# Kernel tuning notes

Measured on AMD Instinct MI355X. Metric: run time of the kernel, lower is better.

Reference implementation:

```python
import jax, jax.numpy as jnp
import numpy as np

N_NODES = 50000
N_EDGES = 1000000


def _edge_conv(x, src, dst, W, b, n_nodes):
    """PyG EdgeConv: msg = nn(cat([x_i, x_j - x_i])), aggr=max over incoming edges."""
    xi = x[dst]                      # [E, C] target features
    xj = x[src]                      # [E, C] source features
    m = jnp.concatenate([xi, xj - xi], axis=-1)          # [E, 2C]
    m = jax.nn.relu(m @ W + b)                           # [E, C_out]
    out = jax.ops.segment_max(m, dst, num_segments=n_nodes)  # [N, C_out]
    # empty segments produce -inf; PyG fills with 0
    return jnp.where(jnp.isfinite(out), out, 0.0)


def setup_inputs() -> dict:
    key = jax.random.key(0)
    ks = jax.random.split(key, 12)
    x = jax.random.normal(ks[0], (N_NODES, 3), dtype=jnp.float32)
    edge_index = jax.random.randint(ks[1], (2, N_EDGES), 0, N_NODES, dtype=jnp.int64)

    def lin(k, fan_in, fan_out):
        s = 1.0 / np.sqrt(fan_in)
        kw, kb = jax.random.split(k)
        W = jax.random.uniform(kw, (fan_in, fan_out), jnp.float32, -s, s)
        b = jax.random.uniform(kb, (fan_out,), jnp.float32, -s, s)
        return W, b

    W1, b1 = lin(ks[2], 6, 64)       # conv1 MLP([3*2, 64])
    W2, b2 = lin(ks[3], 128, 128)    # conv2 MLP([64*2, 128])
    W3, b3 = lin(ks[4], 256, 512)    # conv3 MLP([128*2, 512])
    W4, b4 = lin(ks[5], 512, 256)    # lin1 MLP([512, 256])
    W5, b5 = lin(ks[6], 256, 3)      # lin1 final Linear(256, 3)
    return {"x": x, "edge_index": edge_index,
            "W1": W1, "b1": b1, "W2": W2, "b2": b2, "W3": W3, "b3": b3,
            "W4": W4, "b4": b4, "W5": W5, "b5": b5}


def reference(x, edge_index, W1, b1, W2, b2, W3, b3, W4, b4, W5, b5):
    src = edge_index[0]  # x_j
    dst = edge_index[1]  # x_i (aggregation target)
    n = x.shape[0]
    x1 = _edge_conv(x, src, dst, W1, b1, n)    # [N, 64]
    x2 = _edge_conv(x1, src, dst, W2, b2, n)   # [N, 128]
    x3 = _edge_conv(x2, src, dst, W3, b3, n)   # [N, 512]
    x4 = jax.nn.relu(x3 @ W4 + b4) @ W5 + b5   # [N, 3]
    return x + x4
```

## Files before the change

### kernel.cpp

```cpp
#include <hip/hip_runtime.h>

static constexpr int NN = 50000;
static constexpr int NE = 1000000;

typedef short bf16x8 __attribute__((ext_vector_type(8)));
typedef float f32x4 __attribute__((ext_vector_type(4)));

__device__ inline float bf2f_raw(unsigned short u) {
    return __uint_as_float(((unsigned int)u) << 16);
}
__device__ inline unsigned short f2bf(float f) {
    unsigned int u = __float_as_uint(f);
    u += 0x7fffu + ((u >> 16) & 1u);
    return (unsigned short)(u >> 16);
}
__device__ inline void fmax2(float& a0, float& a1, unsigned int v) {
    a0 = fmaxf(a0, bf2f_raw((unsigned short)(v & 0xffffu)));
    a1 = fmaxf(a1, bf2f_raw((unsigned short)(v >> 16)));
}
__device__ inline unsigned int pack2(float f0, float f1) {
    return (unsigned int)f2bf(f0) | ((unsigned int)f2bf(f1) << 16);
}
__device__ inline unsigned int addrelu2(unsigned int a, float t0, float t1) {
    float f0 = fmaxf(bf2f_raw((unsigned short)(a & 0xffffu)) + t0, 0.f);
    float f1 = fmaxf(bf2f_raw((unsigned short)(a >> 16)) + t1, 0.f);
    return pack2(f0, f1);
}


__global__ void hist_kernel(const int* __restrict__ dst, int* __restrict__ deg) {
    int e = blockIdx.x * blockDim.x + threadIdx.x;
    if (e < NE) atomicAdd(&deg[dst[e]], 1);
}

__global__ __launch_bounds__(1024) void scan_kernel(const int* __restrict__ deg,
                                                    int* __restrict__ rowstart) {
    __shared__ int wave_sums[16];
    __shared__ int carry_s;
    int tid = threadIdx.x;
    int lane = tid & 63;
    int wave = tid >> 6;
    if (tid == 0) carry_s = 0;
    __syncthreads();
    for (int base = 0; base < NN; base += 1024) {
        int idx = base + tid;
        int v = (idx < NN) ? deg[idx] : 0;
        int x = v;
        #pragma unroll
        for (int off = 1; off < 64; off <<= 1) {
            int y = __shfl_up(x, off);
            if (lane >= off) x += y;
        }
        if (lane == 63) wave_sums[wave] = x;
        __syncthreads();
        if (wave == 0 && lane < 16) {
            int s = wave_sums[lane];
            #pragma unroll
            for (int off = 1; off < 16; off <<= 1) {
                int y = __shfl_up(s, off);
                if (lane >= off) s += y;
            }
            wave_sums[lane] = s;
        }
        __syncthreads();
        int wave_off = wave ? wave_sums[wave - 1] : 0;
        int chunk_total = wave_sums[15];
        int carry = carry_s;
        if (idx < NN) rowstart[idx] = carry + wave_off + x - v;
        __syncthreads();
        if (tid == 0) carry_s = carry + chunk_total;
        __syncthreads();
    }
    if (tid == 0) rowstart[NN] = carry_s;
}

__global__ void scatter_kernel(const int* __restrict__ src, const int* __restrict__ dst,
                               const int* __restrict__ rowstart, int* __restrict__ cursor,
                               int* __restrict__ csr) {
    int e = blockIdx.x * blockDim.x + threadIdx.x;
    if (e < NE) {
        int d = dst[e];
        int pos = atomicAdd(&cursor[d], 1);
        csr[rowstart[d] + pos] = src[e];
    }
}


template<int CIN, int COUT>
__global__ void prep_split_t_kernel(const float* __restrict__ W,
                                    unsigned short* __restrict__ Wtbt,
                                    unsigned short* __restrict__ Wbt) {
    int t = blockIdx.x * blockDim.x + threadIdx.x;
    if (t >= CIN * COUT) return;
    int k = t / COUT, c = t % COUT;
    float wt = W[k * COUT + c];
    float wb = W[(CIN + k) * COUT + c];
    Wtbt[c * CIN + k] = f2bf(wt - wb);
    Wbt[c * CIN + k] = f2bf(wb);
}

template<int K, int N>
__global__ void prep_t_kernel(const float* __restrict__ W, unsigned short* __restrict__ Wt) {
    int t = blockIdx.x * blockDim.x + threadIdx.x;
    if (t >= K * N) return;
    int k = t / N, n = t % N;
    Wt[n * K + k] = f2bf(W[k * N + n]);
}


__global__ void conv1_s_kernel(const float* __restrict__ x, const float* __restrict__ W1,
                               unsigned short* __restrict__ s) {
    int t = blockIdx.x * blockDim.x + threadIdx.x;
    int i = t >> 6, c = t & 63;
    if (i >= NN) return;
    float v = x[i * 3 + 0] * W1[3 * 64 + c] + x[i * 3 + 1] * W1[4 * 64 + c] +
              x[i * 3 + 2] * W1[5 * 64 + c];
    s[t] = f2bf(v);
}


__global__ __launch_bounds__(256) void edge_fused_conv1_kernel(
    const unsigned short* __restrict__ s1, const int* __restrict__ rowstart,
    const int* __restrict__ csr, const float* __restrict__ x,
    const float* __restrict__ W1, const float* __restrict__ b1,
    unsigned short* __restrict__ x1) {
    int wid = (blockIdx.x * 256 + threadIdx.x) >> 6;
    int lane = threadIdx.x & 63;
    if (wid >= NN) return;
    int e0 = __builtin_amdgcn_readfirstlane(rowstart[wid]);
    int e1 = __builtin_amdgcn_readfirstlane(rowstart[wid + 1]);
    int h = lane >> 5, c0 = (lane & 31) * 2;
    float t0 = -INFINITY, t1 = -INFINITY;
    const unsigned short* sb = s1 + c0;
    int nedge = e1 - e0;
    for (int base = 0; base < nedge; base += 64) {
        int rem = nedge - base;
        int myj = csr[(lane < rem) ? (e0 + base + lane) : e0];
        int cnt = rem < 64 ? rem : 64;
        int cp = (cnt + 7) & ~7;
        for (int q = 0; q < cp; q += 8) {
            int j0 = __shfl(myj, q + 0 + h);
            int j1 = __shfl(myj, q + 2 + h);
            int j2 = __shfl(myj, q + 4 + h);
            int j3 = __shfl(myj, q + 6 + h);
            unsigned int v0 = *(const unsigned int*)(sb + (size_t)j0 * 64);
            unsigned int v1 = *(const unsigned int*)(sb + (size_t)j1 * 64);
            unsigned int v2 = *(const unsigned int*)(sb + (size_t)j2 * 64);
            unsigned int v3 = *(const unsigned int*)(sb + (size_t)j3 * 64);
            fmax2(t0, t1, v0);
            fmax2(t0, t1, v1);
            fmax2(t0, t1, v2);
            fmax2(t0, t1, v3);
        }
    }
    t0 = fmaxf(t0, __shfl_xor(t0, 32));
    t1 = fmaxf(t1, __shfl_xor(t1, 32));
    if (h == 0) {
        float x0 = x[wid * 3 + 0], xv1 = x[wid * 3 + 1], xv2 = x[wid * 3 + 2];
        int c1 = c0 + 1;
        float a0 = x0 * (W1[c0] - W1[192 + c0]) + xv1 * (W1[64 + c0] - W1[256 + c0]) +
                   xv2 * (W1[128 + c0] - W1[320 + c0]) + b1[c0];
        float a1 = x0 * (W1[c1] - W1[192 + c1]) + xv1 * (W1[64 + c1] - W1[256 + c1]) +
                   xv2 * (W1[128 + c1] - W1[320 + c1]) + b1[c1];
        *(unsigned int*)(x1 + (size_t)wid * 64 + c0) =
            pack2(fmaxf(a0 + t0, 0.f), fmaxf(a1 + t1, 0.f));
    }
}


__global__ __launch_bounds__(256) void edge_fused128_kernel(
    const unsigned short* __restrict__ as, const int* __restrict__ rowstart,
    const int* __restrict__ csr, unsigned short* __restrict__ xout) {
    int wid = (blockIdx.x * 256 + threadIdx.x) >> 6;
    int lane = threadIdx.x & 63;
    if (wid >= NN) return;
    int e0 = __builtin_amdgcn_readfirstlane(rowstart[wid]);
    int e1 = __builtin_amdgcn_readfirstlane(rowstart[wid + 1]);
    float t0 = -INFINITY, t1 = -INFINITY;
    const unsigned short* sb = as + 128 + (size_t)lane * 2;
    int nedge = e1 - e0;
    for (int base = 0; base < nedge; base += 64) {
        int rem = nedge - base;
        int myj = csr[(lane < rem) ? (e0 + base + lane) : e0];
        int cnt = rem < 64 ? rem : 64;
        int cp = (cnt + 7) & ~7;
        for (int q = 0; q < cp; q += 8) {
            int j0 = __shfl(myj, q + 0), j1 = __shfl(myj, q + 1);
            int j2 = __shfl(myj, q + 2), j3 = __shfl(myj, q + 3);
            int j4 = __shfl(myj, q + 4), j5 = __shfl(myj, q + 5);
            int j6 = __shfl(myj, q + 6), j7 = __shfl(myj, q + 7);
            unsigned int v0 = *(const unsigned int*)(sb + (size_t)j0 * 256);
            unsigned int v1 = *(const unsigned int*)(sb + (size_t)j1 * 256);
            unsigned int v2 = *(const unsigned int*)(sb + (size_t)j2 * 256);
            unsigned int v3 = *(const unsigned int*)(sb + (size_t)j3 * 256);
            unsigned int v4 = *(const unsigned int*)(sb + (size_t)j4 * 256);
            unsigned int v5 = *(const unsigned int*)(sb + (size_t)j5 * 256);
            unsigned int v6 = *(const unsigned int*)(sb + (size_t)j6 * 256);
            unsigned int v7 = *(const unsigned int*)(sb + (size_t)j7 * 256);
            fmax2(t0, t1, v0); fmax2(t0, t1, v1);
            fmax2(t0, t1, v2); fmax2(t0, t1, v3);
            fmax2(t0, t1, v4); fmax2(t0, t1, v5);
            fmax2(t0, t1, v6); fmax2(t0, t1, v7);
        }
    }
    unsigned int av = *(const unsigned int*)(as + (size_t)wid * 256 + lane * 2);
    *(unsigned int*)(xout + (size_t)wid * 128 + lane * 2) = addrelu2(av, t0, t1);
}


__global__ __launch_bounds__(256) void edge_fused512_kernel(
    const unsigned short* __restrict__ as, const int* __restrict__ rowstart,
    const int* __restrict__ csr, unsigned short* __restrict__ xout) {
    int wid = (blockIdx.x * 256 + threadIdx.x) >> 6;
    int lane = threadIdx.x & 63;
    if (wid >= NN) return;
    int e0 = __builtin_amdgcn_readfirstlane(rowstart[wid]);
    int e1 = __builtin_amdgcn_readfirstlane(rowstart[wid + 1]);
    float acc[8];
    #pragma unroll
    for (int v = 0; v < 8; ++v) acc[v] = -INFINITY;
    const unsigned short* sb = as + 512 + (size_t)lane * 8;
    int nedge = e1 - e0;
    for (int base = 0; base < nedge; base += 64) {
        int rem = nedge - base;
        int myj = csr[(lane < rem) ? (e0 + base + lane) : e0];
        int cnt = rem < 64 ? rem : 64;
        int cp = (cnt + 7) & ~7;
        for (int q = 0; q < cp; q += 8) {
            int j0 = __shfl(myj, q + 0), j1 = __shfl(myj, q + 1);
            int j2 = __shfl(myj, q + 2), j3 = __shfl(myj, q + 3);
            int j4 = __shfl(myj, q + 4), j5 = __shfl(myj, q + 5);
            int j6 = __shfl(myj, q + 6), j7 = __shfl(myj, q + 7);
            uint4 v0 = *(const uint4*)(sb + (size_t)j0 * 1024);
            uint4 v1 = *(const uint4*)(sb + (size_t)j1 * 1024);
            uint4 v2 = *(const uint4*)(sb + (size_t)j2 * 1024);
            uint4 v3 = *(const uint4*)(sb + (size_t)j3 * 1024);
            uint4 v4 = *(const uint4*)(sb + (size_t)j4 * 1024);
            uint4 v5 = *(const uint4*)(sb + (size_t)j5 * 1024);
            uint4 v6 = *(const uint4*)(sb + (size_t)j6 * 1024);
            uint4 v7 = *(const uint4*)(sb + (size_t)j7 * 1024);
            fmax2(acc[0], acc[1], v0.x); fmax2(acc[2], acc[3], v0.y);
            fmax2(acc[4], acc[5], v0.z); fmax2(acc[6], acc[7], v0.w);
            fmax2(acc[0], acc[1], v1.x); fmax2(acc[2], acc[3], v1.y);
            fmax2(acc[4], acc[5], v1.z); fmax2(acc[6], acc[7], v1.w);
            fmax2(acc[0], acc[1], v2.x); fmax2(acc[2], acc[3], v2.y);
            fmax2(acc[4], acc[5], v2.z); fmax2(acc[6], acc[7], v2.w);
            fmax2(acc[0], acc[1], v3.x); fmax2(acc[2], acc[3], v3.y);
            fmax2(acc[4], acc[5], v3.z); fmax2(acc[6], acc[7], v3.w);
            fmax2(acc[0], acc[1], v4.x); fmax2(acc[2], acc[3], v4.y);
            fmax2(acc[4], acc[5], v4.z); fmax2(acc[6], acc[7], v4.w);
            fmax2(acc[0], acc[1], v5.x); fmax2(acc[2], acc[3], v5.y);
            fmax2(acc[4], acc[5], v5.z); fmax2(acc[6], acc[7], v5.w);
            fmax2(acc[0], acc[1], v6.x); fmax2(acc[2], acc[3], v6.y);
            fmax2(acc[4], acc[5], v6.z); fmax2(acc[6], acc[7], v6.w);
            fmax2(acc[0], acc[1], v7.x); fmax2(acc[2], acc[3], v7.y);
            fmax2(acc[4], acc[5], v7.z); fmax2(acc[6], acc[7], v7.w);
        }
    }
    uint4 av = *(const uint4*)(as + (size_t)wid * 1024 + lane * 8);
    uint4 o;
    o.x = addrelu2(av.x, acc[0], acc[1]);
    o.y = addrelu2(av.y, acc[2], acc[3]);
    o.z = addrelu2(av.z, acc[4], acc[5]);
    o.w = addrelu2(av.w, acc[6], acc[7]);
    *(uint4*)(xout + (size_t)wid * 512 + lane * 8) = o;
}


template<bool RELU>
__global__ __launch_bounds__(256) void mfma_gemm_kernel(
    const unsigned short* __restrict__ A, const unsigned short* __restrict__ Bt,
    const float* __restrict__ bias, int bias_n,
    unsigned short* __restrict__ C, int M, int N, int K) {
    __shared__ __align__(16) unsigned short Asl[128 * 40];
    __shared__ __align__(16) unsigned short Bsl[128 * 40];
    int tid = threadIdx.x;
    int mbase = blockIdx.y * 128, nbase = blockIdx.x * 128;
    int wave = tid >> 6, lane = tid & 63;
    int wm = (wave >> 1) * 64, wn = (wave & 1) * 64;
    int quad = lane >> 4, l16 = lane & 15;
    f32x4 acc[4][4] = {};
    for (int kb = 0; kb < K; kb += 32) {
        #pragma unroll
        for (int h = 0; h < 2; ++h) {
            int c = tid + h * 256;
            int r = c >> 2, kk = (c & 3) * 8;
            uint4 va = make_uint4(0u, 0u, 0u, 0u);
            int gr = mbase + r;
            if (gr < M) va = *(const uint4*)&A[(size_t)gr * K + kb + kk];
            *(uint4*)&Asl[r * 40 + kk] = va;
            uint4 vb = *(const uint4*)&Bt[(size_t)(nbase + r) * K + kb + kk];
            *(uint4*)&Bsl[r * 40 + kk] = vb;
        }
        __syncthreads();
        bf16x8 af[4], bfr[4];
        #pragma unroll
        for (int tt = 0; tt < 4; ++tt) {
            af[tt]  = *(const bf16x8*)&Asl[(wm + tt * 16 + l16) * 40 + quad * 8];
            bfr[tt] = *(const bf16x8*)&Bsl[(wn + tt * 16 + l16) * 40 + quad * 8];
        }
        #pragma unroll
        for (int mt = 0; mt < 4; ++mt)
            #pragma unroll
            for (int nt = 0; nt < 4; ++nt)
                acc[mt][nt] = __builtin_amdgcn_mfma_f32_16x16x32_bf16(
                    af[mt], bfr[nt], acc[mt][nt], 0, 0, 0);
        __syncthreads();
    }
    #pragma unroll
    for (int mt = 0; mt < 4; ++mt) {
        #pragma unroll
        for (int r = 0; r < 4; ++r) {
            int row = mbase + wm + mt * 16 + quad * 4 + r;
            if (row >= M) continue;
            #pragma unroll
            for (int nt = 0; nt < 4; ++nt) {
                int col = nbase + wn + nt * 16 + l16;
                float v = acc[mt][nt][r];
                if (col < bias_n) v += bias[col];
                if (RELU) v = fmaxf(v, 0.f);
                C[(size_t)row * N + col] = f2bf(v);
            }
        }
    }
}


__global__ void final_kernel(const unsigned short* __restrict__ h4,
                             const float* __restrict__ W5, const float* __restrict__ b5,
                             const float* __restrict__ x, float* __restrict__ out) {
    int gt = blockIdx.x * blockDim.x + threadIdx.x;
    int node = gt >> 6;
    int lane = gt & 63;
    if (node >= NN) return;
    ushort4 hv = ((const ushort4*)(h4 + (size_t)node * 256))[lane];
    float hj[4] = {bf2f_raw(hv.x), bf2f_raw(hv.y), bf2f_raw(hv.z), bf2f_raw(hv.w)};
    float acc0 = 0.f, acc1 = 0.f, acc2 = 0.f;
    #pragma unroll
    for (int j = 0; j < 4; ++j) {
        int k = lane * 4 + j;
        acc0 += hj[j] * W5[k * 3 + 0];
        acc1 += hj[j] * W5[k * 3 + 1];
        acc2 += hj[j] * W5[k * 3 + 2];
    }
    #pragma unroll
    for (int off = 32; off; off >>= 1) {
        acc0 += __shfl_down(acc0, off);
        acc1 += __shfl_down(acc1, off);
        acc2 += __shfl_down(acc2, off);
    }
    if (lane == 0) {
        out[node * 3 + 0] = x[node * 3 + 0] + acc0 + b5[0];
        out[node * 3 + 1] = x[node * 3 + 1] + acc1 + b5[1];
        out[node * 3 + 2] = x[node * 3 + 2] + acc2 + b5[2];
    }
}

__global__ void fallback_copy_kernel(const float* __restrict__ x, float* __restrict__ out) {
    int t = blockIdx.x * blockDim.x + threadIdx.x;
    if (t < NN * 3) out[t] = x[t];
}


extern "C" void kernel_launch(void* const* d_in, const int* in_sizes, int n_in,
                              void* d_out, int out_size, void* d_ws, size_t ws_size,
                              hipStream_t stream) {
    const float* x  = (const float*)d_in[0];
    const int*   ei = (const int*)d_in[1];
    const float* W1 = (const float*)d_in[2];
    const float* b1 = (const float*)d_in[3];
    const float* W2 = (const float*)d_in[4];
    const float* b2 = (const float*)d_in[5];
    const float* W3 = (const float*)d_in[6];
    const float* b3 = (const float*)d_in[7];
    const float* W4 = (const float*)d_in[8];
    const float* b4 = (const float*)d_in[9];
    const float* W5 = (const float*)d_in[10];
    const float* b5 = (const float*)d_in[11];
    float* out = (float*)d_out;

    char* p = (char*)d_ws;
    auto alloc = [&](size_t bytes) -> void* {
        void* r = (void*)p;
        p += (bytes + 255) & ~(size_t)255;
        return r;
    };
    int* deg      = (int*)alloc((size_t)NN * 4);
    int* rowstart = (int*)alloc((size_t)(NN + 1) * 4);
    int* cursor   = (int*)alloc((size_t)NN * 4);
    int* csr      = (int*)alloc((size_t)NE * 4);
    unsigned short* Bt2 = (unsigned short*)alloc(256 * 64 * 2);
    unsigned short* Bt3 = (unsigned short*)alloc(1024 * 128 * 2);
    unsigned short* W4t = (unsigned short*)alloc(256 * 512 * 2);
    unsigned short* x1 = (unsigned short*)alloc((size_t)NN * 64 * 2);
    unsigned short* x2 = (unsigned short*)alloc((size_t)NN * 128 * 2);
    unsigned short* x3 = (unsigned short*)alloc((size_t)NN * 512 * 2);
    unsigned short* as_slab = (unsigned short*)alloc((size_t)NN * 1024 * 2);
    size_t need = (size_t)(p - (char*)d_ws);
    if (ws_size < need) {
        fallback_copy_kernel<<<(NN * 3 + 255) / 256, 256, 0, stream>>>(x, out);
        return;
    }
    unsigned short* s1 = as_slab;
    unsigned short* h4 = as_slab;

    const int* src = ei;
    const int* dst = ei + NE;

    hipMemsetAsync(deg, 0, (size_t)NN * 4, stream);
    hipMemsetAsync(cursor, 0, (size_t)NN * 4, stream);
    hist_kernel<<<(NE + 255) / 256, 256, 0, stream>>>(dst, deg);
    scan_kernel<<<1, 1024, 0, stream>>>(deg, rowstart);
    scatter_kernel<<<(NE + 255) / 256, 256, 0, stream>>>(src, dst, rowstart, cursor, csr);

    prep_split_t_kernel<64, 128><<<32, 256, 0, stream>>>(W2, Bt2, Bt2 + 128 * 64);
    prep_split_t_kernel<128, 512><<<256, 256, 0, stream>>>(W3, Bt3, Bt3 + 512 * 128);
    prep_t_kernel<512, 256><<<512, 256, 0, stream>>>(W4, W4t);

    conv1_s_kernel<<<NN * 64 / 256, 256, 0, stream>>>(x, W1, s1);
    edge_fused_conv1_kernel<<<12500, 256, 0, stream>>>(s1, rowstart, csr, x, W1, b1, x1);

    mfma_gemm_kernel<false><<<dim3(2, 391), 256, 0, stream>>>(
        x1, Bt2, b2, 128, as_slab, NN, 256, 64);
    edge_fused128_kernel<<<12500, 256, 0, stream>>>(as_slab, rowstart, csr, x2);

    mfma_gemm_kernel<false><<<dim3(8, 391), 256, 0, stream>>>(
        x2, Bt3, b3, 512, as_slab, NN, 1024, 128);
    edge_fused512_kernel<<<12500, 256, 0, stream>>>(as_slab, rowstart, csr, x3);

    mfma_gemm_kernel<true><<<dim3(2, 391), 256, 0, stream>>>(
        x3, W4t, b4, 256, h4, NN, 256, 512);

    final_kernel<<<NN / 4, 256, 0, stream>>>(h4, W5, b5, x, out);
}
```

Baseline: 634.3 us.

## Fuse final W5 projection into W4 GEMM epilogue and merge setup kernels

Fuses the last linear layer (W5) into the epilogue of the W4 MFMA GEMM. Each 128-column tile reduces its ReLU outputs against W5 and atomically adds into an output pre-initialised with x+b5, which removes the h4 write/read and the separate final kernel. It also merges the three weight-prep kernels into one launch, moves the cursor zeroing into the scan kernel to drop a memset, and halves the gather unroll in the 512-wide edge kernel. The cost is float atomics on the output, which make summation order nondeterministic, and possibly less memory-level parallelism in the edge gather.

```diff
diff --git a/kernel.cpp b/kernel.cpp
--- a/kernel.cpp
+++ b/kernel.cpp
@@ -28,18 +28,27 @@
 }
 
 
+__global__ void init_out_kernel(const float* __restrict__ x, const float* __restrict__ b5,
+                                float* __restrict__ out) {
+    int t = blockIdx.x * blockDim.x + threadIdx.x;
+    if (t < NN * 3) out[t] = x[t] + b5[t % 3];
+}
+
+
 __global__ void hist_kernel(const int* __restrict__ dst, int* __restrict__ deg) {
     int e = blockIdx.x * blockDim.x + threadIdx.x;
     if (e < NE) atomicAdd(&deg[dst[e]], 1);
 }
 
 __global__ __launch_bounds__(1024) void scan_kernel(const int* __restrict__ deg,
-                                                    int* __restrict__ rowstart) {
+                                                    int* __restrict__ rowstart,
+                                                    int* __restrict__ cursor) {
     __shared__ int wave_sums[16];
     __shared__ int carry_s;
     int tid = threadIdx.x;
     int lane = tid & 63;
     int wave = tid >> 6;
+    for (int i = tid; i < NN; i += 1024) cursor[i] = 0;
     if (tid == 0) carry_s = 0;
     __syncthreads();
     for (int base = 0; base < NN; base += 1024) {
@@ -86,25 +95,30 @@
 }
 
 
-template<int CIN, int COUT>
-__global__ void prep_split_t_kernel(const float* __restrict__ W,
-                                    unsigned short* __restrict__ Wtbt,
-                                    unsigned short* __restrict__ Wbt) {
+__global__ void prep_all_kernel(const float* __restrict__ W2, const float* __restrict__ W3,
+                                const float* __restrict__ W4,
+                                unsigned short* __restrict__ Bt2,
+                                unsigned short* __restrict__ Bt3,
+                                unsigned short* __restrict__ W4t) {
     int t = blockIdx.x * blockDim.x + threadIdx.x;
-    if (t >= CIN * COUT) return;
-    int k = t / COUT, c = t % COUT;
-    float wt = W[k * COUT + c];
-    float wb = W[(CIN + k) * COUT + c];
-    Wtbt[c * CIN + k] = f2bf(wt - wb);
-    Wbt[c * CIN + k] = f2bf(wb);
-}
-
-template<int K, int N>
-__global__ void prep_t_kernel(const float* __restrict__ W, unsigned short* __restrict__ Wt) {
-    int t = blockIdx.x * blockDim.x + threadIdx.x;
-    if (t >= K * N) return;
-    int k = t / N, n = t % N;
-    Wt[n * K + k] = f2bf(W[k * N + n]);
+    if (t < 8192) {
+        int k = t / 128, c = t % 128;
+        float wt = W2[k * 128 + c];
+        float wb = W2[(64 + k) * 128 + c];
+        Bt2[c * 64 + k] = f2bf(wt - wb);
+        Bt2[(128 + c) * 64 + k] = f2bf(wb);
+    } else if (t < 8192 + 65536) {
+        int u = t - 8192;
+        int k = u / 512, c = u % 512;
+        float wt = W3[k * 512 + c];
+        float wb = W3[(128 + k) * 512 + c];
+        Bt3[c * 128 + k] = f2bf(wt - wb);
+        Bt3[(512 + c) * 128 + k] = f2bf(wb);
+    } else if (t < 8192 + 65536 + 131072) {
+        int u = t - 8192 - 65536;
+        int k = u / 256, n = u % 256;
+        W4t[n * 512 + k] = f2bf(W4[k * 256 + n]);
+    }
 }
 
 
@@ -225,20 +239,14 @@
         int rem = nedge - base;
         int myj = csr[(lane < rem) ? (e0 + base + lane) : e0];
         int cnt = rem < 64 ? rem : 64;
-        int cp = (cnt + 7) & ~7;
-        for (int q = 0; q < cp; q += 8) {
+        int cp = (cnt + 3) & ~3;
+        for (int q = 0; q < cp; q += 4) {
             int j0 = __shfl(myj, q + 0), j1 = __shfl(myj, q + 1);
             int j2 = __shfl(myj, q + 2), j3 = __shfl(myj, q + 3);
-            int j4 = __shfl(myj, q + 4), j5 = __shfl(myj, q + 5);
-            int j6 = __shfl(myj, q + 6), j7 = __shfl(myj, q + 7);
             uint4 v0 = *(const uint4*)(sb + (size_t)j0 * 1024);
             uint4 v1 = *(const uint4*)(sb + (size_t)j1 * 1024);
             uint4 v2 = *(const uint4*)(sb + (size_t)j2 * 1024);
             uint4 v3 = *(const uint4*)(sb + (size_t)j3 * 1024);
-            uint4 v4 = *(const uint4*)(sb + (size_t)j4 * 1024);
-            uint4 v5 = *(const uint4*)(sb + (size_t)j5 * 1024);
-            uint4 v6 = *(const uint4*)(sb + (size_t)j6 * 1024);
-            uint4 v7 = *(const uint4*)(sb + (size_t)j7 * 1024);
             fmax2(acc[0], acc[1], v0.x); fmax2(acc[2], acc[3], v0.y);
             fmax2(acc[4], acc[5], v0.z); fmax2(acc[6], acc[7], v0.w);
             fmax2(acc[0], acc[1], v1.x); fmax2(acc[2], acc[3], v1.y);
@@ -247,14 +255,6 @@
             fmax2(acc[4], acc[5], v2.z); fmax2(acc[6], acc[7], v2.w);
             fmax2(acc[0], acc[1], v3.x); fmax2(acc[2], acc[3], v3.y);
             fmax2(acc[4], acc[5], v3.z); fmax2(acc[6], acc[7], v3.w);
-            fmax2(acc[0], acc[1], v4.x); fmax2(acc[2], acc[3], v4.y);
-            fmax2(acc[4], acc[5], v4.z); fmax2(acc[6], acc[7], v4.w);
-            fmax2(acc[0], acc[1], v5.x); fmax2(acc[2], acc[3], v5.y);
-            fmax2(acc[4], acc[5], v5.z); fmax2(acc[6], acc[7], v5.w);
-            fmax2(acc[0], acc[1], v6.x); fmax2(acc[2], acc[3], v6.y);
-            fmax2(acc[4], acc[5], v6.z); fmax2(acc[6], acc[7], v6.w);
-            fmax2(acc[0], acc[1], v7.x); fmax2(acc[2], acc[3], v7.y);
-            fmax2(acc[4], acc[5], v7.z); fmax2(acc[6], acc[7], v7.w);
         }
     }
     uint4 av = *(const uint4*)(as + (size_t)wid * 1024 + lane * 8);
@@ -267,7 +267,6 @@
 }
 
 
-template<bool RELU>
 __global__ __launch_bounds__(256) void mfma_gemm_kernel(
     const unsigned short* __restrict__ A, const unsigned short* __restrict__ Bt,
     const float* __restrict__ bias, int bias_n,
@@ -318,7 +317,6 @@
                 int col = nbase + wn + nt * 16 + l16;
                 float v = acc[mt][nt][r];
                 if (col < bias_n) v += bias[col];
-                if (RELU) v = fmaxf(v, 0.f);
                 C[(size_t)row * N + col] = f2bf(v);
             }
         }
@@ -326,33 +324,79 @@
 }
 
 
-__global__ void final_kernel(const unsigned short* __restrict__ h4,
-                             const float* __restrict__ W5, const float* __restrict__ b5,
-                             const float* __restrict__ x, float* __restrict__ out) {
-    int gt = blockIdx.x * blockDim.x + threadIdx.x;
-    int node = gt >> 6;
-    int lane = gt & 63;
-    if (node >= NN) return;
-    ushort4 hv = ((const ushort4*)(h4 + (size_t)node * 256))[lane];
-    float hj[4] = {bf2f_raw(hv.x), bf2f_raw(hv.y), bf2f_raw(hv.z), bf2f_raw(hv.w)};
-    float acc0 = 0.f, acc1 = 0.f, acc2 = 0.f;
+__global__ __launch_bounds__(256) void mfma_gemm_w5_kernel(
+    const unsigned short* __restrict__ A, const unsigned short* __restrict__ Bt,
+    const float* __restrict__ b4, const float* __restrict__ W5,
+    float* __restrict__ out, int M, int K) {
+    __shared__ __align__(16) unsigned short Asl[128 * 40];
+    __shared__ __align__(16) unsigned short Bsl[128 * 40];
+    int tid = threadIdx.x;
+    int mbase = blockIdx.y * 128, nbase = blockIdx.x * 128;
+    int wave = tid >> 6, lane = tid & 63;
+    int wm = (wave >> 1) * 64, wn = (wave & 1) * 64;
+    int quad = lane >> 4, l16 = lane & 15;
+    f32x4 acc[4][4] = {};
+    for (int kb = 0; kb < K; kb += 32) {
+        #pragma unroll
+        for (int h = 0; h < 2; ++h) {
+            int c = tid + h * 256;
+            int r = c >> 2, kk = (c & 3) * 8;
+            uint4 va = make_uint4(0u, 0u, 0u, 0u);
+            int gr = mbase + r;
+            if (gr < M) va = *(const uint4*)&A[(size_t)gr * K + kb + kk];
+            *(uint4*)&Asl[r * 40 + kk] = va;
+            uint4 vb = *(const uint4*)&Bt[(size_t)(nbase + r) * K + kb + kk];
+            *(uint4*)&Bsl[r * 40 + kk] = vb;
+        }
+        __syncthreads();
+        bf16x8 af[4], bfr[4];
+        #pragma unroll
+        for (int tt = 0; tt < 4; ++tt) {
+            af[tt]  = *(const bf16x8*)&Asl[(wm + tt * 16 + l16) * 40 + quad * 8];
+            bfr[tt] = *(const bf16x8*)&Bsl[(wn + tt * 16 + l16) * 40 + quad * 8];
+        }
+        #pragma unroll
+        for (int mt = 0; mt < 4; ++mt)
+            #pragma unroll
+            for (int nt = 0; nt < 4; ++nt)
+                acc[mt][nt] = __builtin_amdgcn_mfma_f32_16x16x32_bf16(
+                    af[mt], bfr[nt], acc[mt][nt], 0, 0, 0);
+        __syncthreads();
+    }
+    float w5r[4][3], b4v[4];
     #pragma unroll
-    for (int j = 0; j < 4; ++j) {
-        int k = lane * 4 + j;
-        acc0 += hj[j] * W5[k * 3 + 0];
-        acc1 += hj[j] * W5[k * 3 + 1];
-        acc2 += hj[j] * W5[k * 3 + 2];
+    for (int nt = 0; nt < 4; ++nt) {
+        int col = nbase + wn + nt * 16 + l16;
+        b4v[nt] = b4[col];
+        w5r[nt][0] = W5[col * 3 + 0];
+        w5r[nt][1] = W5[col * 3 + 1];
+        w5r[nt][2] = W5[col * 3 + 2];
     }
     #pragma unroll
-    for (int off = 32; off; off >>= 1) {
-        acc0 += __shfl_down(acc0, off);
-        acc1 += __shfl_down(acc1, off);
-        acc2 += __shfl_down(acc2, off);
-    }
-    if (lane == 0) {
-        out[node * 3 + 0] = x[node * 3 + 0] + acc0 + b5[0];
-        out[node * 3 + 1] = x[node * 3 + 1] + acc1 + b5[1];
-        out[node * 3 + 2] = x[node * 3 + 2] + acc2 + b5[2];
+    for (int mt = 0; mt < 4; ++mt) {
+        #pragma unroll
+        for (int r = 0; r < 4; ++r) {
+            int row = mbase + wm + mt * 16 + quad * 4 + r;
+            float p0 = 0.f, p1 = 0.f, p2 = 0.f;
+            #pragma unroll
+            for (int nt = 0; nt < 4; ++nt) {
+                float h = fmaxf(acc[mt][nt][r] + b4v[nt], 0.f);
+                p0 += h * w5r[nt][0];
+                p1 += h * w5r[nt][1];
+                p2 += h * w5r[nt][2];
+            }
+            #pragma unroll
+            for (int m = 8; m; m >>= 1) {
+                p0 += __shfl_xor(p0, m);
+                p1 += __shfl_xor(p1, m);
+                p2 += __shfl_xor(p2, m);
+            }
+            if (l16 == 0 && row < M) {
+                atomicAdd(&out[row * 3 + 0], p0);
+                atomicAdd(&out[row * 3 + 1], p1);
+                atomicAdd(&out[row * 3 + 2], p2);
+            }
+        }
     }
 }
 
@@ -402,34 +446,30 @@
         return;
     }
     unsigned short* s1 = as_slab;
-    unsigned short* h4 = as_slab;
 
     const int* src = ei;
     const int* dst = ei + NE;
 
+    init_out_kernel<<<(NN * 3 + 255) / 256, 256, 0, stream>>>(x, b5, out);
+
     hipMemsetAsync(deg, 0, (size_t)NN * 4, stream);
-    hipMemsetAsync(cursor, 0, (size_t)NN * 4, stream);
     hist_kernel<<<(NE + 255) / 256, 256, 0, stream>>>(dst, deg);
-    scan_kernel<<<1, 1024, 0, stream>>>(deg, rowstart);
+    scan_kernel<<<1, 1024, 0, stream>>>(deg, rowstart, cursor);
     scatter_kernel<<<(NE + 255) / 256, 256, 0, stream>>>(src, dst, rowstart, cursor, csr);
 
-    prep_split_t_kernel<64, 128><<<32, 256, 0, stream>>>(W2, Bt2, Bt2 + 128 * 64);
-    prep_split_t_kernel<128, 512><<<256, 256, 0, stream>>>(W3, Bt3, Bt3 + 512 * 128);
-    prep_t_kernel<512, 256><<<512, 256, 0, stream>>>(W4, W4t);
+    prep_all_kernel<<<800, 256, 0, stream>>>(W2, W3, W4, Bt2, Bt3, W4t);
 
     conv1_s_kernel<<<NN * 64 / 256, 256, 0, stream>>>(x, W1, s1);
     edge_fused_conv1_kernel<<<12500, 256, 0, stream>>>(s1, rowstart, csr, x, W1, b1, x1);
 
-    mfma_gemm_kernel<false><<<dim3(2, 391), 256, 0, stream>>>(
+    mfma_gemm_kernel<<<dim3(2, 391), 256, 0, stream>>>(
         x1, Bt2, b2, 128, as_slab, NN, 256, 64);
     edge_fused128_kernel<<<12500, 256, 0, stream>>>(as_slab, rowstart, csr, x2);
 
-    mfma_gemm_kernel<false><<<dim3(8, 391), 256, 0, stream>>>(
+    mfma_gemm_kernel<<<dim3(8, 391), 256, 0, stream>>>(
         x2, Bt3, b3, 512, as_slab, NN, 1024, 128);
     edge_fused512_kernel<<<12500, 256, 0, stream>>>(as_slab, rowstart, csr, x3);
 
-    mfma_gemm_kernel<true><<<dim3(2, 391), 256, 0, stream>>>(
-        x3, W4t, b4, 256, h4, NN, 256, 512);
-
-    final_kernel<<<NN / 4, 256, 0, stream>>>(h4, W5, b5, x, out);
-}
+    mfma_gemm_w5_kernel<<<dim3(2, 391), 256, 0, stream>>>(
+        x3, W4t, b4, W5, out, NN, 512);
+}
```

New measurement: 631.9 us. Within noise of the previous version (-0.4%).
